# Kernel tuning notes

Hardware: AMD Instinct MI355X
Metric: run time of the kernel (lower is better)

## Reference

```python
import jax, jax.numpy as jnp
import numpy as np

B, S, D = 4, 2048, 1024
EPS = 1e-5


def setup_inputs() -> dict:
    key = jax.random.key(0)
    ks = jax.random.split(key, 8)
    s = 1.0 / np.sqrt(D)
    return {
        "x": jax.random.normal(ks[0], (B, S, D), dtype=jnp.float32),
        "Wq": jax.random.normal(ks[1], (D, D), dtype=jnp.float32) * s,
        "Wk": jax.random.normal(ks[2], (D, D), dtype=jnp.float32) * s,
        "Wv": jax.random.normal(ks[3], (D, D), dtype=jnp.float32) * s,
        "W1": jax.random.normal(ks[4], (D, D), dtype=jnp.float32) * s,
        "b1": jnp.zeros((D,), dtype=jnp.float32),
        "W2": jax.random.normal(ks[5], (D, D), dtype=jnp.float32) * s,
        "b2": jnp.zeros((D,), dtype=jnp.float32),
        "gamma": jnp.ones((D,), dtype=jnp.float32),
        "beta": jnp.zeros((D,), dtype=jnp.float32),
    }


def _layer_norm(x, gamma, beta):
    mu = jnp.mean(x, axis=-1, keepdims=True)
    var = jnp.mean(jnp.square(x - mu), axis=-1, keepdims=True)
    return (x - mu) * jax.lax.rsqrt(var + EPS) * gamma + beta


def reference(x, Wq, Wk, Wv, W1, b1, W2, b2, gamma, beta):
    seq_len, d = x.shape[1], x.shape[2]
    # torch Linear: y = x @ W.T
    Q = jnp.einsum('bsd,ed->bse', x, Wq)
    K = jnp.einsum('bsd,ed->bse', x, Wk)
    V = jnp.einsum('bsd,ed,->bse', x, Wv, jnp.float32(1.0)) if False else jnp.einsum('bsd,ed->bse', x, Wv)
    scores = jnp.einsum('bqd,bkd->bqk', Q, K) / jnp.sqrt(jnp.float32(d))
    causal = jnp.tril(jnp.ones((seq_len, seq_len), dtype=bool))  # [S,S]
    scores = jnp.where(causal[None, :, :], scores, -jnp.inf)
    attn = jax.nn.softmax(scores, axis=-1)
    attn_out = jnp.einsum('bqk,bkd->bqd', attn, V)
    # dropout is identity at eval
    h = _layer_norm(x + attn_out, gamma, beta)
    ff = jnp.einsum('bsd,ed->bse', jax.nn.relu(jnp.einsum('bsd,ed->bse', h, W1) + b1), W2) + b2
    out = _layer_norm(h + ff, gamma, beta)
    return out
```

## Files before the change

### kernel.cpp

```cpp
#include <hip/hip_runtime.h>
#include <math.h>
#include <cstdint>
#include <cstddef>

#define DI __device__ __forceinline__

typedef __bf16 bf16x8 __attribute__((ext_vector_type(8)));
typedef float f32x4 __attribute__((ext_vector_type(4)));

static constexpr int kB = 4, kS = 2048, kD = 1024;
static constexpr int kM = kB * kS;
static constexpr float kScale = 0.03125f;
static constexpr float kEps = 1e-5f;

DI unsigned short f2bf(float f) {
  unsigned u = __float_as_uint(f);
  u += 0x7FFFu + ((u >> 16) & 1u);
  return (unsigned short)(u >> 16);
}
DI float bf2f(unsigned short h) {
  return __uint_as_float(((unsigned)h) << 16);
}

DI void gld_lds16(const void* g, void* l) {
  __builtin_amdgcn_global_load_lds(
      (__attribute__((address_space(1))) void*)(void*)g,
      (__attribute__((address_space(3))) void*)l, 16, 0, 0);
}

__global__ __launch_bounds__(256) void k_cast_all(
    const float* __restrict__ x, const float* __restrict__ Wq,
    const float* __restrict__ Wk, const float* __restrict__ Wv,
    const float* __restrict__ W1, const float* __restrict__ W2,
    unsigned short* __restrict__ xb, unsigned short* __restrict__ Wqkb,
    unsigned short* __restrict__ Wvb, unsigned short* __restrict__ W1b,
    unsigned short* __restrict__ W2b) {
  const int i = blockIdx.x * 256 + threadIdx.x;
  const int X4 = kM * kD / 4;
  const int W4 = kD * kD / 4;
  const float* src;
  unsigned short* dst;
  int j;
  if (i < X4) { src = x; dst = xb; j = i; }
  else if (i < X4 + W4)     { src = Wq; dst = Wqkb;          j = i - X4; }
  else if (i < X4 + 2 * W4) { src = Wk; dst = Wqkb + 4 * W4; j = i - X4 - W4; }
  else if (i < X4 + 3 * W4) { src = Wv; dst = Wvb;           j = i - X4 - 2 * W4; }
  else if (i < X4 + 4 * W4) { src = W1; dst = W1b;           j = i - X4 - 3 * W4; }
  else                      { src = W2; dst = W2b;           j = i - X4 - 4 * W4; }
  float4 v = ((const float4*)src)[j];
  ushort4 o;
  o.x = f2bf(v.x); o.y = f2bf(v.y); o.z = f2bf(v.z); o.w = f2bf(v.w);
  ((ushort4*)dst)[j] = o;
}

template <int OUT_BF16, int RELU, int CAUSAL>
__global__ __launch_bounds__(256, 2) void k_gemm_nt(
    const unsigned short* __restrict__ A, const unsigned short* __restrict__ B,
    void* __restrict__ Cv, const float* __restrict__ bias,
    int M, int N, int K, int lda, int ldb, int ldc,
    long sA, long sB, long sC) {
  int bm, bn;
  {
    int lin = blockIdx.x + gridDim.x * blockIdx.y;
    const int nblk = gridDim.x * gridDim.y;
    if (CAUSAL != 2 && (nblk & 7) == 0)
      lin = (lin & 7) * (nblk >> 3) + (lin >> 3);
    if (CAUSAL == 1) {
      const int t = lin;
      int r = (int)floorf((sqrtf(8.f * (float)t + 1.f) - 1.f) * 0.5f);
      while ((r + 1) * (r + 2) / 2 <= t) ++r;
      while (r * (r + 1) / 2 > t) --r;
      bm = r * 128;
      bn = (t - r * (r + 1) / 2) * 128;
    } else if (CAUSAL == 2) {
      bm = (gridDim.y - 1 - blockIdx.y) * 128;
      bn = blockIdx.x * 128;
    } else {
      bm = (lin / gridDim.x) * 128;
      bn = (lin % gridDim.x) * 128;
    }
  }
  A += (long)blockIdx.z * sA;
  B += (long)blockIdx.z * sB;
  const int Keff = (CAUSAL == 2) ? ((K < bm + 128) ? K : bm + 128) : K;

  const int tid = threadIdx.x;
  const int lane = tid & 63;
  const int wm = ((tid >> 6) >> 1) * 64;
  const int wn = ((tid >> 6) & 1) * 64;

  __shared__ __align__(16) unsigned short Asm[128 * 64];
  __shared__ __align__(16) unsigned short Bsm[128 * 64];

  f32x4 acc[4][4];
#pragma unroll
  for (int i = 0; i < 4; ++i)
#pragma unroll
    for (int j = 0; j < 4; ++j) acc[i][j] = (f32x4){0.f, 0.f, 0.f, 0.f};

  const int r_row = tid >> 3;
  const int dst_k = (tid & 7) * 8;
  const int src_k = ((tid & 7) ^ ((tid >> 3) & 7)) * 8;
  const int fm = lane & 15;
  const int fq = lane >> 4;

  for (int k0 = 0; k0 < Keff; k0 += 64) {
#pragma unroll
    for (int i = 0; i < 4; ++i) {
      const int row = i * 32 + r_row;
      gld_lds16(A + (long)(bm + row) * lda + (k0 + src_k), Asm + row * 64 + dst_k);
      gld_lds16(B + (long)(bn + row) * ldb + (k0 + src_k), Bsm + row * 64 + dst_k);
    }
    __syncthreads();
#pragma unroll
    for (int kk = 0; kk < 2; ++kk) {
      bf16x8 af[4], bfr[4];
#pragma unroll
      for (int i = 0; i < 4; ++i) {
        const int pa = ((kk * 4 + fq) ^ (fm & 7)) * 8;
        af[i]  = *(const bf16x8*)(Asm + (wm + i * 16 + fm) * 64 + pa);
        bfr[i] = *(const bf16x8*)(Bsm + (wn + i * 16 + fm) * 64 + pa);
      }
#pragma unroll
      for (int i = 0; i < 4; ++i)
#pragma unroll
        for (int j = 0; j < 4; ++j)
          acc[i][j] = __builtin_amdgcn_mfma_f32_16x16x32_bf16(af[i], bfr[j], acc[i][j], 0, 0, 0);
    }
    __syncthreads();
  }

  const long cb = (long)blockIdx.z * sC;
#pragma unroll
  for (int i = 0; i < 4; ++i) {
#pragma unroll
    for (int j = 0; j < 4; ++j) {
      const int col = bn + wn + j * 16 + fm;
      const float bv = bias ? bias[col] : 0.f;
#pragma unroll
      for (int r = 0; r < 4; ++r) {
        const int row = bm + wm + i * 16 + fq * 4 + r;
        float v = acc[i][j][r] + bv;
        if (RELU) v = fmaxf(v, 0.f);
        if (OUT_BF16)
          ((unsigned short*)Cv)[cb + (long)row * ldc + col] = f2bf(v);
        else
          ((float*)Cv)[cb + (long)row * ldc + col] = v;
      }
    }
  }
}

DI float wsum(float v) {
  v += __shfl_xor(v, 32, 64);
  v += __shfl_xor(v, 16, 64);
  v += __shfl_xor(v, 8, 64);
  v += __shfl_xor(v, 4, 64);
  v += __shfl_xor(v, 2, 64);
  v += __shfl_xor(v, 1, 64);
  return v;
}
DI float wmax(float v) {
  v = fmaxf(v, __shfl_xor(v, 32, 64));
  v = fmaxf(v, __shfl_xor(v, 16, 64));
  v = fmaxf(v, __shfl_xor(v, 8, 64));
  v = fmaxf(v, __shfl_xor(v, 4, 64));
  v = fmaxf(v, __shfl_xor(v, 2, 64));
  v = fmaxf(v, __shfl_xor(v, 1, 64));
  return v;
}

__global__ __launch_bounds__(256) void k_softmax_causal(
    const unsigned short* __restrict__ S, unsigned short* __restrict__ P) {
  const int row = blockIdx.x;
  const int q = row & (kS - 1);
  const int lim = (q & ~127) + 128;
  const unsigned short* Srow = S + (long)row * kS;
  unsigned short* Prow = P + (long)row * kS;
  const int tid = threadIdx.x;
  __shared__ float red[4];

  float v[8];
  float mx = -INFINITY;
#pragma unroll
  for (int i = 0; i < 8; ++i) {
    const int k = tid + i * 256;
    float xv = -INFINITY;
    if (k <= q) xv = bf2f(Srow[k]) * kScale;
    v[i] = xv;
    mx = fmaxf(mx, xv);
  }
  mx = wmax(mx);
  if ((tid & 63) == 0) red[tid >> 6] = mx;
  __syncthreads();
  mx = fmaxf(fmaxf(red[0], red[1]), fmaxf(red[2], red[3]));
  __syncthreads();

  float sum = 0.f;
#pragma unroll
  for (int i = 0; i < 8; ++i) {
    const float e = (v[i] > -INFINITY) ? __expf(v[i] - mx) : 0.f;
    v[i] = e;
    sum += e;
  }
  sum = wsum(sum);
  if ((tid & 63) == 0) red[tid >> 6] = sum;
  __syncthreads();
  sum = red[0] + red[1] + red[2] + red[3];
  const float inv = 1.f / sum;
#pragma unroll
  for (int i = 0; i < 8; ++i) {
    const int k = tid + i * 256;
    if (k < lim) Prow[k] = f2bf(v[i] * inv);
  }
}

template <int WRITE_BF16>
__global__ __launch_bounds__(256) void k_residual_ln(
    const float* __restrict__ X, const unsigned short* __restrict__ Yb,
    const float* __restrict__ gamma, const float* __restrict__ beta,
    float* __restrict__ Out, unsigned short* __restrict__ OutB) {
  const long base = (long)blockIdx.x * kD;
  const int tid = threadIdx.x;
  __shared__ float reds[4], redss[4];
  float v[4];
  float s = 0.f, ss2 = 0.f;
#pragma unroll
  for (int i = 0; i < 4; ++i) {
    const int k = tid + i * 256;
    const float xv = X[base + k] + bf2f(Yb[base + k]);
    v[i] = xv;
    s += xv;
    ss2 += xv * xv;
  }
  s = wsum(s);
  ss2 = wsum(ss2);
  if ((tid & 63) == 0) { reds[tid >> 6] = s; redss[tid >> 6] = ss2; }
  __syncthreads();
  s = reds[0] + reds[1] + reds[2] + reds[3];
  ss2 = redss[0] + redss[1] + redss[2] + redss[3];
  const float mu = s * (1.f / kD);
  float var = ss2 * (1.f / kD) - mu * mu;
  var = fmaxf(var, 0.f);
  const float rstd = rsqrtf(var + kEps);
#pragma unroll
  for (int i = 0; i < 4; ++i) {
    const int k = tid + i * 256;
    const float y = (v[i] - mu) * rstd * gamma[k] + beta[k];
    Out[base + k] = y;
    if (WRITE_BF16) OutB[base + k] = f2bf(y);
  }
}

extern "C" void kernel_launch(void* const* d_in, const int* in_sizes, int n_in,
                              void* d_out, int out_size, void* d_ws, size_t ws_size,
                              hipStream_t stream) {
  (void)in_sizes; (void)n_in; (void)out_size; (void)ws_size;
  const float* x     = (const float*)d_in[0];
  const float* Wq    = (const float*)d_in[1];
  const float* Wk    = (const float*)d_in[2];
  const float* Wv    = (const float*)d_in[3];
  const float* W1    = (const float*)d_in[4];
  const float* b1    = (const float*)d_in[5];
  const float* W2    = (const float*)d_in[6];
  const float* b2    = (const float*)d_in[7];
  const float* gamma = (const float*)d_in[8];
  const float* beta  = (const float*)d_in[9];
  float* out = (float*)d_out;

  char* base = (char*)d_ws;
  size_t off = 0;
  auto alloc = [&](size_t bytes) -> void* {
    void* p = base + off;
    off = (off + bytes + 255) & ~(size_t)255;
    return p;
  };

  unsigned short* xb     = (unsigned short*)alloc((size_t)kM * kD * 2);
  unsigned short* Wqkb   = (unsigned short*)alloc((size_t)2 * kD * kD * 2);
  unsigned short* Wvb    = (unsigned short*)alloc((size_t)kD * kD * 2);
  unsigned short* W1b    = (unsigned short*)alloc((size_t)kD * kD * 2);
  unsigned short* W2b    = (unsigned short*)alloc((size_t)kD * kD * 2);
  unsigned short* QKb    = (unsigned short*)alloc((size_t)kM * 2 * kD * 2);
  unsigned short* Vt     = (unsigned short*)alloc((size_t)kM * kD * 2);
  unsigned short* Sb     = (unsigned short*)alloc((size_t)kB * kS * kS * 2);
  unsigned short* Pb     = (unsigned short*)alloc((size_t)kB * kS * kS * 2);
  unsigned short* attn_b = (unsigned short*)alloc((size_t)kM * kD * 2);
  float*          h      = (float*)alloc((size_t)kM * kD * 4);
  unsigned short* ff_b = attn_b;
  unsigned short* hb   = Sb;
  unsigned short* mid  = Pb;

  dim3 blk(256);

  {
    const int n4 = (kM * kD + 5 * kD * kD) / 4;
    k_cast_all<<<n4 / 256, blk, 0, stream>>>(x, Wq, Wk, Wv, W1, W2,
                                             xb, Wqkb, Wvb, W1b, W2b);
  }

  k_gemm_nt<1, 0, 0><<<dim3(2 * kD / 128, kM / 128, 1), blk, 0, stream>>>(
      xb, Wqkb, QKb, nullptr, kM, 2 * kD, kD, kD, kD, 2 * kD, 0, 0, 0);

  k_gemm_nt<1, 0, 0><<<dim3(kS / 128, kD / 128, kB), blk, 0, stream>>>(
      Wvb, xb, Vt, nullptr, kD, kS, kD, kD, kD, kS,
      0, (long)kS * kD, (long)kD * kS);

  k_gemm_nt<1, 0, 1><<<dim3(136, 1, kB), blk, 0, stream>>>(
      QKb, QKb + kD, Sb, nullptr, kS, kS, kD, 2 * kD, 2 * kD, kS,
      (long)kS * 2 * kD, (long)kS * 2 * kD, (long)kS * kS);

  k_softmax_causal<<<kM, blk, 0, stream>>>(Sb, Pb);

  k_gemm_nt<1, 0, 2><<<dim3(kD / 128, kS / 128, kB), blk, 0, stream>>>(
      Pb, Vt, attn_b, nullptr, kS, kD, kS, kS, kS, kD,
      (long)kS * kS, (long)kD * kS, (long)kS * kD);

  k_residual_ln<1><<<kM, blk, 0, stream>>>(x, attn_b, gamma, beta, h, hb);

  k_gemm_nt<1, 1, 0><<<dim3(kD / 128, kM / 128, 1), blk, 0, stream>>>(
      hb, W1b, mid, b1, kM, kD, kD, kD, kD, kD, 0, 0, 0);
  k_gemm_nt<1, 0, 0><<<dim3(kD / 128, kM / 128, 1), blk, 0, stream>>>(
      mid, W2b, ff_b, b2, kM, kD, kD, kD, kD, kD, 0, 0, 0);

  k_residual_ln<0><<<kM, blk, 0, stream>>>(h, ff_b, gamma, beta, out, nullptr);
}
```

Baseline: 347.6 us.

## Pair causal PV row tiles per block and drop fp32 LN intermediate

Replaces the causal P·V GEMM with a dedicated kernel in which each block computes two mirrored row tiles (hi and lo), so every block does the same total K work and shares the V tile loads between them. This balances the triangular workload and halves the block count. The first residual LayerNorm now writes only a bf16 h, and the second LayerNorm reads that bf16 h, removing an fp32 intermediate write and read. The trade-off is lower precision in the residual path, plus higher register and LDS pressure with one block per CU.

```diff
diff --git a/kernel.cpp b/kernel.cpp
--- a/kernel.cpp
+++ b/kernel.cpp
@@ -63,7 +63,7 @@
   {
     int lin = blockIdx.x + gridDim.x * blockIdx.y;
     const int nblk = gridDim.x * gridDim.y;
-    if (CAUSAL != 2 && (nblk & 7) == 0)
+    if ((nblk & 7) == 0)
       lin = (lin & 7) * (nblk >> 3) + (lin >> 3);
     if (CAUSAL == 1) {
       const int t = lin;
@@ -72,9 +72,6 @@
       while (r * (r + 1) / 2 > t) --r;
       bm = r * 128;
       bn = (t - r * (r + 1) / 2) * 128;
-    } else if (CAUSAL == 2) {
-      bm = (gridDim.y - 1 - blockIdx.y) * 128;
-      bn = blockIdx.x * 128;
     } else {
       bm = (lin / gridDim.x) * 128;
       bn = (lin % gridDim.x) * 128;
@@ -82,7 +79,6 @@
   }
   A += (long)blockIdx.z * sA;
   B += (long)blockIdx.z * sB;
-  const int Keff = (CAUSAL == 2) ? ((K < bm + 128) ? K : bm + 128) : K;
 
   const int tid = threadIdx.x;
   const int lane = tid & 63;
@@ -104,7 +100,7 @@
   const int fm = lane & 15;
   const int fq = lane >> 4;
 
-  for (int k0 = 0; k0 < Keff; k0 += 64) {
+  for (int k0 = 0; k0 < K; k0 += 64) {
 #pragma unroll
     for (int i = 0; i < 4; ++i) {
       const int row = i * 32 + r_row;
@@ -151,6 +147,100 @@
   }
 }
 
+__global__ __launch_bounds__(256, 1) void k_attn_pv(
+    const unsigned short* __restrict__ P, const unsigned short* __restrict__ Vt,
+    unsigned short* __restrict__ O) {
+  const int y = blockIdx.y;
+  const int bn = blockIdx.x * 128;
+  const int bm_hi = (15 - y) * 128;
+  const int bm_lo = y * 128;
+  const int Khi = bm_hi + 128;
+  const int Klo = bm_lo + 128;
+  P  += (long)blockIdx.z * kS * kS;
+  Vt += (long)blockIdx.z * kD * kS;
+  O  += (long)blockIdx.z * kS * kD;
+
+  const int tid = threadIdx.x;
+  const int lane = tid & 63;
+  const int wm = ((tid >> 6) >> 1) * 64;
+  const int wn = ((tid >> 6) & 1) * 64;
+
+  __shared__ __align__(16) unsigned short Ah[128 * 64];
+  __shared__ __align__(16) unsigned short Al[128 * 64];
+  __shared__ __align__(16) unsigned short Bs[128 * 64];
+
+  f32x4 ah[4][4], al[4][4];
+#pragma unroll
+  for (int i = 0; i < 4; ++i)
+#pragma unroll
+    for (int j = 0; j < 4; ++j) {
+      ah[i][j] = (f32x4){0.f, 0.f, 0.f, 0.f};
+      al[i][j] = (f32x4){0.f, 0.f, 0.f, 0.f};
+    }
+
+  const int r_row = tid >> 3;
+  const int dst_k = (tid & 7) * 8;
+  const int src_k = ((tid & 7) ^ ((tid >> 3) & 7)) * 8;
+  const int fm = lane & 15;
+  const int fq = lane >> 4;
+
+  for (int k0 = 0; k0 < Khi; k0 += 64) {
+    const bool lo = (k0 < Klo);
+#pragma unroll
+    for (int i = 0; i < 4; ++i) {
+      const int row = i * 32 + r_row;
+      gld_lds16(Vt + (long)(bn + row) * kS + (k0 + src_k), Bs + row * 64 + dst_k);
+      gld_lds16(P + (long)(bm_hi + row) * kS + (k0 + src_k), Ah + row * 64 + dst_k);
+      if (lo)
+        gld_lds16(P + (long)(bm_lo + row) * kS + (k0 + src_k), Al + row * 64 + dst_k);
+    }
+    __syncthreads();
+#pragma unroll
+    for (int kk = 0; kk < 2; ++kk) {
+      bf16x8 afh[4], bfr[4];
+#pragma unroll
+      for (int i = 0; i < 4; ++i) {
+        const int pa = ((kk * 4 + fq) ^ (fm & 7)) * 8;
+        afh[i] = *(const bf16x8*)(Ah + (wm + i * 16 + fm) * 64 + pa);
+        bfr[i] = *(const bf16x8*)(Bs + (wn + i * 16 + fm) * 64 + pa);
+      }
+#pragma unroll
+      for (int i = 0; i < 4; ++i)
+#pragma unroll
+        for (int j = 0; j < 4; ++j)
+          ah[i][j] = __builtin_amdgcn_mfma_f32_16x16x32_bf16(afh[i], bfr[j], ah[i][j], 0, 0, 0);
+      if (lo) {
+        bf16x8 afl[4];
+#pragma unroll
+        for (int i = 0; i < 4; ++i) {
+          const int pa = ((kk * 4 + fq) ^ (fm & 7)) * 8;
+          afl[i] = *(const bf16x8*)(Al + (wm + i * 16 + fm) * 64 + pa);
+        }
+#pragma unroll
+        for (int i = 0; i < 4; ++i)
+#pragma unroll
+          for (int j = 0; j < 4; ++j)
+            al[i][j] = __builtin_amdgcn_mfma_f32_16x16x32_bf16(afl[i], bfr[j], al[i][j], 0, 0, 0);
+      }
+    }
+    __syncthreads();
+  }
+
+#pragma unroll
+  for (int i = 0; i < 4; ++i) {
+#pragma unroll
+    for (int j = 0; j < 4; ++j) {
+      const int col = bn + wn + j * 16 + fm;
+#pragma unroll
+      for (int r = 0; r < 4; ++r) {
+        const int rr = wm + i * 16 + fq * 4 + r;
+        O[(long)(bm_hi + rr) * kD + col] = f2bf(ah[i][j][r]);
+        O[(long)(bm_lo + rr) * kD + col] = f2bf(al[i][j][r]);
+      }
+    }
+  }
+}
+
 DI float wsum(float v) {
   v += __shfl_xor(v, 32, 64);
   v += __shfl_xor(v, 16, 64);
@@ -215,9 +305,9 @@
   }
 }
 
-template <int WRITE_BF16>
+template <int X_BF16, int OUT_FP32>
 __global__ __launch_bounds__(256) void k_residual_ln(
-    const float* __restrict__ X, const unsigned short* __restrict__ Yb,
+    const void* __restrict__ Xv, const unsigned short* __restrict__ Yb,
     const float* __restrict__ gamma, const float* __restrict__ beta,
     float* __restrict__ Out, unsigned short* __restrict__ OutB) {
   const long base = (long)blockIdx.x * kD;
@@ -228,7 +318,9 @@
 #pragma unroll
   for (int i = 0; i < 4; ++i) {
     const int k = tid + i * 256;
-    const float xv = X[base + k] + bf2f(Yb[base + k]);
+    const float xf = X_BF16 ? bf2f(((const unsigned short*)Xv)[base + k])
+                            : ((const float*)Xv)[base + k];
+    const float xv = xf + bf2f(Yb[base + k]);
     v[i] = xv;
     s += xv;
     ss2 += xv * xv;
@@ -247,8 +339,8 @@
   for (int i = 0; i < 4; ++i) {
     const int k = tid + i * 256;
     const float y = (v[i] - mu) * rstd * gamma[k] + beta[k];
-    Out[base + k] = y;
-    if (WRITE_BF16) OutB[base + k] = f2bf(y);
+    if (OUT_FP32) Out[base + k] = y;
+    else          OutB[base + k] = f2bf(y);
   }
 }
 
@@ -286,7 +378,6 @@
   unsigned short* Sb     = (unsigned short*)alloc((size_t)kB * kS * kS * 2);
   unsigned short* Pb     = (unsigned short*)alloc((size_t)kB * kS * kS * 2);
   unsigned short* attn_b = (unsigned short*)alloc((size_t)kM * kD * 2);
-  float*          h      = (float*)alloc((size_t)kM * kD * 4);
   unsigned short* ff_b = attn_b;
   unsigned short* hb   = Sb;
   unsigned short* mid  = Pb;
@@ -312,16 +403,16 @@
 
   k_softmax_causal<<<kM, blk, 0, stream>>>(Sb, Pb);
 
-  k_gemm_nt<1, 0, 2><<<dim3(kD / 128, kS / 128, kB), blk, 0, stream>>>(
-      Pb, Vt, attn_b, nullptr, kS, kD, kS, kS, kS, kD,
-      (long)kS * kS, (long)kD * kS, (long)kS * kD);
-
-  k_residual_ln<1><<<kM, blk, 0, stream>>>(x, attn_b, gamma, beta, h, hb);
+  k_attn_pv<<<dim3(kD / 128, 8, kB), blk, 0, stream>>>(Pb, Vt, attn_b);
+
+  k_residual_ln<0, 0><<<kM, blk, 0, stream>>>(x, attn_b, gamma, beta,
+                                              nullptr, hb);
 
   k_gemm_nt<1, 1, 0><<<dim3(kD / 128, kM / 128, 1), blk, 0, stream>>>(
       hb, W1b, mid, b1, kM, kD, kD, kD, kD, kD, 0, 0, 0);
   k_gemm_nt<1, 0, 0><<<dim3(kD / 128, kM / 128, 1), blk, 0, stream>>>(
       mid, W2b, ff_b, b2, kM, kD, kD, kD, kD, kD, 0, 0, 0);
 
-  k_residual_ln<0><<<kM, blk, 0, stream>>>(h, ff_b, gamma, beta, out, nullptr);
-}
+  k_residual_ln<1, 1><<<kM, blk, 0, stream>>>(hb, ff_b, gamma, beta,
+                                              out, nullptr);
+}
```

Measured after the change: 342.2 us. No clear change (-1.6%).
